# Kernel optimization log

Measured on AMD Instinct MI355X. Metric: run time of the kernel, lower is better.

## Reference

```python
import jax, jax.numpy as jnp
import numpy as np

B, M, K = 8, 2048, 2048
LAMBDA_VEL, LAMBDA_SURV, LAMBDA_OT = 1.0, 1.0, 0.1
REG_OT, REG_MASS, NUM_ITER_DIFF = 0.05, 1.0, 5


def setup_inputs() -> dict:
    key = jax.random.key(0)
    k0, k1, k2, k3, k4, k5 = jax.random.split(key, 6)
    return {
        "x_0": jax.random.normal(k0, (B, M, 3), jnp.float32),
        "x_gt": jax.random.normal(k1, (B, K, 3), jnp.float32),
        "v_pred": jax.random.normal(k2, (B, M, 3), jnp.float32),
        "alpha_pred": jax.random.normal(k3, (B, M, 1), jnp.float32),
        "t": jax.random.uniform(k4, (B, 1), jnp.float32),
        "matched_x_gt_precomputed": jax.random.normal(k5, (B, M, 3), jnp.float32),
    }


def _sinkhorn_unbalanced_log(log_a, log_b, K_log, tau, num_iter):
    # log_a: (B,M), log_b: (B,K), K_log: (B,M,K)
    log_u = jnp.zeros_like(log_a)
    log_v = jnp.zeros_like(log_b)
    for _ in range(num_iter):  # small fixed iteration count
        log_Kv = jax.nn.logsumexp(K_log + log_v[:, None, :], axis=2)   # (B,M)
        log_u = tau * (log_a - log_Kv)
        log_KTu = jax.nn.logsumexp(K_log + log_u[:, :, None], axis=1)  # (B,K)
        log_v = tau * (log_b - log_KTu)
    return jnp.exp(log_u[:, :, None] + K_log + log_v[:, None, :])      # pi (B,M,K)


def reference(x_0, x_gt, v_pred, alpha_pred, t, matched_x_gt_precomputed):
    sg = jax.lax.stop_gradient
    src = sg(x_0)   # (B,M,3)
    tgt = sg(x_gt)  # (B,K,3)

    # squared euclidean cost via gemm form (matches torch.cdist(p=2)**2)
    s2 = jnp.sum(src * src, axis=-1)  # (B,M)
    t2 = jnp.sum(tgt * tgt, axis=-1)  # (B,K)
    cost = s2[:, :, None] + t2[:, None, :] - 2.0 * jnp.einsum("bmd,bkd->bmk", src, tgt)
    cost = jnp.maximum(cost, 0.0)
    cost = cost / (jnp.max(cost, axis=(1, 2), keepdims=True) + 1e-8)

    # differentiable source marginal from survival logits
    alpha_soft = 10.0 * jnp.tanh(alpha_pred[..., 0] / 10.0)  # (B,M)
    a = jax.nn.sigmoid(alpha_soft)
    b = jnp.broadcast_to(jnp.sum(a, axis=1, keepdims=True) / K, (a.shape[0], K))

    tau = REG_MASS / (REG_MASS + REG_OT)
    log_a = jnp.log(jnp.maximum(a, 1e-30))
    log_b = jnp.log(jnp.maximum(b, 1e-30))
    K_log = -cost / REG_OT

    pi = _sinkhorn_unbalanced_log(log_a, log_b, K_log, tau, NUM_ITER_DIFF)  # (B,M,K)
    surv = jnp.sum(pi, axis=2)  # (B,M)
    surv_norm = jnp.clip(surv / (a + 1e-8), 0.0, 1.0)[..., None]  # (B,M,1)

    # velocity head
    v_target = sg(matched_x_gt_precomputed - x_0)
    weights = sg(jax.nn.sigmoid(alpha_pred))[..., 0]  # (B,M)
    sq_err = jnp.sum((v_pred - v_target) ** 2, axis=-1)
    loss_vel = jnp.sum(sq_err * weights) / jnp.maximum(jnp.sum(weights), 1.0)

    # survival head: BCE-with-logits, mean reduction
    x = alpha_pred
    y = sg(surv_norm)
    bce = jnp.maximum(x, 0.0) - x * y + jnp.log1p(jnp.exp(-jnp.abs(x)))
    loss_surv = jnp.mean(bce)

    # transport-cost head (differentiable through pi)
    loss_transport = jnp.sum(pi * sg(cost)) / jnp.maximum(jnp.sum(pi), 1e-8)

    return LAMBDA_VEL * loss_vel + LAMBDA_SURV * loss_surv + LAMBDA_OT * loss_transport
```

## Files before the change

### kernel.cpp

```cpp
#include <hip/hip_runtime.h>
#include <math.h>


#define LOG2E 1.4426950408889634f
#define TAU   0.95238095238095238f
#define NEG20LOG2E (-28.853900817779268f)

typedef float v2f __attribute__((ext_vector_type(2)));

enum : int {
  OFF_LU    = 0,
  OFF_LV    = 16384,
  OFF_CPART = 32768,
  OFF_SUMAP = 33280,
  OFF_SWP   = 33792,
  OFF_SEWP  = 34304,
  OFF_FPART = 34816,
  OFF_BBAR  = 36352,
  OFF_TAIL  = 40448,
  OFF_END   = 40480
};

__device__ __forceinline__ float fexp2(float x){ return __builtin_amdgcn_exp2f(x); }
__device__ __forceinline__ float flog2(float x){ return __builtin_amdgcn_logf(x); }

__device__ __forceinline__ float ld3(const float* p){
  return __hip_atomic_load(p, __ATOMIC_RELAXED, __HIP_MEMORY_SCOPE_AGENT);
}
__device__ __forceinline__ void st3(float* p, float v){
  __hip_atomic_store(p, v, __ATOMIC_RELAXED, __HIP_MEMORY_SCOPE_AGENT);
}

__device__ __forceinline__ float wave_sum(float v){
  #pragma unroll
  for(int m=32;m;m>>=1) v += __shfl_xor(v,m,64);
  return v;
}
__device__ __forceinline__ float wave_max(float v){
  #pragma unroll
  for(int m=32;m;m>>=1) v = fmaxf(v,__shfl_xor(v,m,64));
  return v;
}

__device__ __forceinline__ void bbar(unsigned* bbase, int phase, int blk){
  __syncthreads();
  if(threadIdx.x == 0){
    asm volatile("s_waitcnt vmcnt(0)" ::: "memory");
    const int g = (blk>>4)&3;
    unsigned* garr = bbase + g*32;
    unsigned* root = bbase + 4*32;
    unsigned* grel = bbase + (8+g)*32;
    const unsigned va = __hip_atomic_fetch_add(garr, 1u, __ATOMIC_RELAXED,
                                               __HIP_MEMORY_SCOPE_AGENT);
    if(va == (unsigned)(16*phase - 1)){
      const unsigned vr = __hip_atomic_fetch_add(root, 1u, __ATOMIC_RELAXED,
                                                 __HIP_MEMORY_SCOPE_AGENT);
      if(vr == (unsigned)(4*phase - 1)){
        #pragma unroll
        for(int g2=0; g2<4; ++g2)
          __hip_atomic_store(bbase + (8+g2)*32, (unsigned)phase,
                             __ATOMIC_RELAXED, __HIP_MEMORY_SCOPE_AGENT);
      }
    }
    while(__hip_atomic_load(grel, __ATOMIC_RELAXED, __HIP_MEMORY_SCOPE_AGENT)
          < (unsigned)phase)
      __builtin_amdgcn_s_sleep(1);
    asm volatile("" ::: "memory");
  }
  __syncthreads();
}

__global__ __launch_bounds__(256) void k_init(float* ws){
  unsigned* bar = reinterpret_cast<unsigned*>(ws);
  for(int i=threadIdx.x; i<OFF_END-OFF_BBAR; i+=256) bar[OFF_BBAR+i] = 0u;
}

#define LSE_PASS(ROWV, FIRSTV, PH) {                                          \
    const float4* sPT = ROWV ? sB : sA;                                       \
    float* lo = ws + (ROWV?OFF_LV:OFF_LU) + 2048*b;                           \
    float* op = ws + (ROWV?OFF_LU:OFF_LV);                                    \
    const float4 A0=ROWV?AR[0]:AC[0], A1=ROWV?AR[1]:AC[1],                    \
                 A2=ROWV?AR[2]:AC[2], A3=ROWV?AR[3]:AC[3];                    \
    if(!FIRSTV){                                                              \
      for(int i=tid;i<2048;i+=512) sL[i] = ld3(lo+i) + sPT[i].w;              \
    }                                                                         \
    __syncthreads();                                                          \
    const v2f ax01={A0.x,A1.x}, ay01={A0.y,A1.y}, az01={A0.z,A1.z};           \
    const v2f ax23={A2.x,A3.x}, ay23={A2.y,A3.y}, az23={A2.z,A3.z};           \
    v2f s01={0.0f,0.0f}, s23={0.0f,0.0f};                                     \
    _Pragma("unroll 2")                                                       \
    for(int k=lane;k<2048;k+=64){                                             \
      const float4 pt = sPT[k];                                               \
      const float wk = FIRSTV ? pt.w : sL[k];                                 \
      const v2f px={pt.x,pt.x}, py={pt.y,pt.y}, pz={pt.z,pt.z}, pw={wk,wk};   \
      const v2f c01 = __builtin_elementwise_fma(ax01,px,                      \
                      __builtin_elementwise_fma(ay01,py,                      \
                      __builtin_elementwise_fma(az01,pz,pw)));                \
      const v2f c23 = __builtin_elementwise_fma(ax23,px,                      \
                      __builtin_elementwise_fma(ay23,py,                      \
                      __builtin_elementwise_fma(az23,pz,pw)));                \
      s01 += (v2f){fexp2(c01.x), fexp2(c01.y)};                               \
      s23 += (v2f){fexp2(c23.x), fexp2(c23.y)};                               \
    }                                                                         \
    const float s0=wave_sum(s01.x), s1=wave_sum(s01.y);                       \
    const float s2=wave_sum(s23.x), s3=wave_sum(s23.y);                       \
    if(lane==0){                                                              \
      st3(op+r0g  , TAU*((ROWV?la[0]:lb2) - fmaf(sc,A0.w,flog2(s0))));        \
      st3(op+r0g+1, TAU*((ROWV?la[1]:lb2) - fmaf(sc,A1.w,flog2(s1))));        \
      st3(op+r0g+2, TAU*((ROWV?la[2]:lb2) - fmaf(sc,A2.w,flog2(s2))));        \
      st3(op+r0g+3, TAU*((ROWV?la[3]:lb2) - fmaf(sc,A3.w,flog2(s3))));        \
    }                                                                         \
    bbar(bbase, PH, blk);                                                     \
  }

__global__ __launch_bounds__(512,4) void k_fused(const float* __restrict__ x0,
                                                 const float* __restrict__ xgt,
                                                 const float* __restrict__ vp,
                                                 const float* __restrict__ ap,
                                                 const float* __restrict__ mxp,
                                                 float* __restrict__ ws,
                                                 float* __restrict__ out){
  __shared__ float4 sA[2048];
  __shared__ float4 sB[2048];
  __shared__ float  sL[2048];
  __shared__ float  sa32[32], sla[32], sal[32];
  __shared__ float  sred[24];
  __shared__ int    sLast;
  const int blk = blockIdx.x, tid = threadIdx.x, lane = tid&63, wid = tid>>6;
  const int b = blk>>6, j = blk&63;
  const int r0l = j*32 + (wid<<2);
  const int r0g = b*2048 + r0l;
  unsigned* bbase = reinterpret_cast<unsigned*>(ws) + OFF_BBAR + b*512;

  for(int i=tid;i<2048;i+=512){
    const int gi = (b*2048 + i)*3;
    const float x = x0[gi], y = x0[gi+1], z = x0[gi+2];
    sA[i] = make_float4(x,y,z, x*x+y*y+z*z);
    const float gx = xgt[gi], gy = xgt[gi+1], gz = xgt[gi+2];
    sB[i] = make_float4(gx,gy,gz, gx*gx+gy*gy+gz*gz);
  }
  if(wid == 0){
    float a_=0.0f, w_=0.0f, se_=0.0f;
    if(lane < 32){
      const int row = b*2048 + j*32 + lane;
      const float al = ap[row];
      const float a = 1.0f/(1.0f + fexp2(-10.0f*tanhf(al*0.1f)*LOG2E));
      sa32[lane] = a;
      sla[lane]  = flog2(fmaxf(a,1e-30f));
      sal[lane]  = al;
      const float w = 1.0f/(1.0f + fexp2(-al*LOG2E));
      const float x = x0[row*3], y = x0[row*3+1], z = x0[row*3+2];
      const float tx = mxp[row*3]-x, ty = mxp[row*3+1]-y, tz = mxp[row*3+2]-z;
      const float dx = vp[row*3]-tx, dy = vp[row*3+1]-ty, dz = vp[row*3+2]-tz;
      a_ = a; w_ = w; se_ = (dx*dx+dy*dy+dz*dz)*w;
    }
    const float sa_s = wave_sum(a_), sw_s = wave_sum(w_), sew_s = wave_sum(se_);
    if(lane == 0){
      st3(ws+OFF_SUMAP+blk, sa_s);
      st3(ws+OFF_SWP  +blk, sw_s);
      st3(ws+OFF_SEWP +blk, sew_s);
    }
  }
  __syncthreads();

  float4 AR[4], AC[4]; float la[4], av[4], alv[4];
  #pragma unroll
  for(int r=0;r<4;r++){
    AR[r] = sA[r0l+r]; AC[r] = sB[r0l+r];
    la[r] = sla[(wid<<2)+r]; av[r] = sa32[(wid<<2)+r]; alv[r] = sal[(wid<<2)+r];
  }

  {
    float c0=0,c1=0,c2=0,c3=0;
    #pragma unroll 2
    for(int k=lane;k<2048;k+=64){
      const float4 pt = sB[k];
      float d;
      d = AR[0].x*pt.x+AR[0].y*pt.y+AR[0].z*pt.z; c0=fmaxf(c0, AR[0].w+pt.w-2.0f*d);
      d = AR[1].x*pt.x+AR[1].y*pt.y+AR[1].z*pt.z; c1=fmaxf(c1, AR[1].w+pt.w-2.0f*d);
      d = AR[2].x*pt.x+AR[2].y*pt.y+AR[2].z*pt.z; c2=fmaxf(c2, AR[2].w+pt.w-2.0f*d);
      d = AR[3].x*pt.x+AR[3].y*pt.y+AR[3].z*pt.z; c3=fmaxf(c3, AR[3].w+pt.w-2.0f*d);
    }
    const float cmv = wave_max(fmaxf(fmaxf(c0,c1),fmaxf(c2,c3)));
    if(lane==0) sred[wid] = cmv;
    __syncthreads();
    if(tid==0){
      float m = sred[0];
      #pragma unroll
      for(int i=1;i<8;i++) m = fmaxf(m, sred[i]);
      st3(ws+OFF_CPART+blk, m);
    }
  }
  bbar(bbase, 1, blk);

  const float cm = wave_max(ld3(ws+OFF_CPART + b*64 + lane));
  const float sc = NEG20LOG2E/(cm + 1e-8f);
  const float n2sc = -2.0f*sc;
  const float sav = wave_sum(ld3(ws+OFF_SUMAP + b*64 + lane));
  const float lb2 = flog2(fmaxf(sav*(1.0f/2048.0f), 1e-30f));

  for(int i=tid;i<2048;i+=512){
    const float4 qa = sA[i];
    sA[i] = make_float4(n2sc*qa.x, n2sc*qa.y, n2sc*qa.z, sc*qa.w);
    const float4 qb = sB[i];
    sB[i] = make_float4(n2sc*qb.x, n2sc*qb.y, n2sc*qb.z, sc*qb.w);
  }
  __syncthreads();

  LSE_PASS(true,  true,  2)
  LSE_PASS(false, false, 3)
  LSE_PASS(true,  false, 4)
  LSE_PASS(false, false, 5)
  LSE_PASS(true,  false, 6)
  LSE_PASS(false, false, 7)
  LSE_PASS(true,  false, 8)
  LSE_PASS(false, false, 9)
  LSE_PASS(true,  false, 10)
  LSE_PASS(false, false, 11)

  {
    float* lv = ws + OFF_LV + 2048*b;
    for(int i=tid;i<2048;i+=512) sL[i] = ld3(lv+i);
    __syncthreads();
    const float lu0=ld3(ws+OFF_LU+r0g),   lu1=ld3(ws+OFF_LU+r0g+1);
    const float lu2=ld3(ws+OFF_LU+r0g+2), lu3=ld3(ws+OFF_LU+r0g+3);
    const v2f ax01={AR[0].x,AR[1].x}, ay01={AR[0].y,AR[1].y}, az01={AR[0].z,AR[1].z};
    const v2f ax23={AR[2].x,AR[3].x}, ay23={AR[2].y,AR[3].y}, az23={AR[2].z,AR[3].z};
    v2f S01={0.0f,0.0f},S23={0.0f,0.0f};
    v2f Q01={0.0f,0.0f},Q23={0.0f,0.0f};
    v2f L01={0.0f,0.0f},L23={0.0f,0.0f};
    #pragma unroll 2
    for(int k=lane;k<2048;k+=64){
      const float4 pt = sB[k];
      const float lvk = sL[k];
      const float wk = pt.w + lvk;
      const v2f px={pt.x,pt.x}, py={pt.y,pt.y}, pz={pt.z,pt.z}, pw={wk,wk};
      const v2f lk={lvk,lvk};
      const v2f c01 = __builtin_elementwise_fma(ax01,px,
                      __builtin_elementwise_fma(ay01,py,
                      __builtin_elementwise_fma(az01,pz,pw)));
      const v2f c23 = __builtin_elementwise_fma(ax23,px,
                      __builtin_elementwise_fma(ay23,py,
                      __builtin_elementwise_fma(az23,pz,pw)));
      const v2f p01 = {fexp2(c01.x), fexp2(c01.y)};
      const v2f p23 = {fexp2(c23.x), fexp2(c23.y)};
      S01 += p01;                      S23 += p23;
      Q01 = __builtin_elementwise_fma(p01,c01,Q01);
      Q23 = __builtin_elementwise_fma(p23,c23,Q23);
      L01 = __builtin_elementwise_fma(p01,lk,L01);
      L23 = __builtin_elementwise_fma(p23,lk,L23);
    }
    float S[4]={wave_sum(S01.x),wave_sum(S01.y),wave_sum(S23.x),wave_sum(S23.y)};
    float Q[4]={wave_sum(Q01.x),wave_sum(Q01.y),wave_sum(Q23.x),wave_sum(Q23.y)};
    float L[4]={wave_sum(L01.x),wave_sum(L01.y),wave_sum(L23.x),wave_sum(L23.y)};
    const float lus[4]={lu0,lu1,lu2,lu3};
    float spc = 0.0f, bce = 0.0f, spt = 0.0f;
    #pragma unroll
    for(int r=0;r<4;r++){
      const float cr = fmaf(sc, AR[r].w, lus[r]);
      const float p2 = fexp2(cr);
      const float sp = p2*S[r];
      spc += p2*fmaf(cr,S[r],Q[r]) - p2*L[r] - lus[r]*sp;
      float yv = sp / (av[r] + 1e-8f);
      yv = fminf(fmaxf(yv,0.0f),1.0f);
      const float al = alv[r];
      bce += fmaxf(al,0.0f) - al*yv
           + 0.69314718056f*flog2(1.0f + fexp2(-fabsf(al)*LOG2E));
      spt += sp;
    }
    if(lane==0){ sred[wid]=bce; sred[8+wid]=spt; sred[16+wid]=spc; }
    __syncthreads();
    if(tid==0){
      float tb=0, ts=0, tc=0;
      #pragma unroll
      for(int i=0;i<8;i++){ tb+=sred[i]; ts+=sred[8+i]; tc+=sred[16+i]; }
      st3(ws+OFF_FPART +        blk, tb);
      st3(ws+OFF_FPART + 512  + blk, ts);
      st3(ws+OFF_FPART + 1024 + blk, tc);
    }
  }

  __syncthreads();
  if(tid == 0){
    asm volatile("s_waitcnt vmcnt(0)" ::: "memory");
    unsigned* tail = reinterpret_cast<unsigned*>(ws) + OFF_TAIL;
    const unsigned v = __hip_atomic_fetch_add(tail, 1u, __ATOMIC_RELAXED,
                                              __HIP_MEMORY_SCOPE_AGENT);
    sLast = (v == 511u) ? 1 : 0;
  }
  __syncthreads();
  if(sLast){
    float pb = ld3(ws+OFF_FPART+tid);
    float ps = ld3(ws+OFF_FPART+512+tid);
    float pc = ld3(ws+OFF_FPART+1024+tid);
    float pw = ld3(ws+OFF_SWP+tid);
    float pe = ld3(ws+OFF_SEWP+tid);
    pb=wave_sum(pb); ps=wave_sum(ps); pc=wave_sum(pc);
    pw=wave_sum(pw); pe=wave_sum(pe);
    if(lane==0){
      sL[wid*5+0]=pb; sL[wid*5+1]=ps; sL[wid*5+2]=pc;
      sL[wid*5+3]=pw; sL[wid*5+4]=pe;
    }
    __syncthreads();
    if(tid==0){
      float bce=0, sp=0, spc=0, sw=0, sew=0;
      #pragma unroll
      for(int w=0;w<8;w++){
        bce+=sL[w*5+0]; sp+=sL[w*5+1]; spc+=sL[w*5+2];
        sw +=sL[w*5+3]; sew+=sL[w*5+4];
      }
      const float loss_vel  = sew / fmaxf(sw, 1.0f);
      const float loss_surv = bce / 16384.0f;
      const float loss_tr = (spc * (-0.03465735902799726f)) / fmaxf(sp, 1e-8f);
      out[0] = loss_vel + loss_surv + 0.1f*loss_tr;
    }
  }
}

extern "C" void kernel_launch(void* const* d_in, const int* in_sizes, int n_in,
                              void* d_out, int out_size, void* d_ws, size_t ws_size,
                              hipStream_t stream) {
  (void)in_sizes; (void)n_in; (void)out_size; (void)ws_size;
  const float* x0  = (const float*)d_in[0];
  const float* xgt = (const float*)d_in[1];
  const float* vp  = (const float*)d_in[2];
  const float* ap  = (const float*)d_in[3];
  const float* mxp = (const float*)d_in[5];
  float* ws  = (float*)d_ws;
  float* out = (float*)d_out;

  k_init<<<1, 256, 0, stream>>>(ws);

  k_fused<<<512, 512, 0, stream>>>(x0, xgt, vp, ap, mxp, ws, out);
}
```

Before: 108.8 us.

## Switch shared point storage to SoA pairs and vectorize over columns

```diff
diff --git a/kernel.cpp b/kernel.cpp
--- a/kernel.cpp
+++ b/kernel.cpp
@@ -23,6 +23,9 @@
 
 __device__ __forceinline__ float fexp2(float x){ return __builtin_amdgcn_exp2f(x); }
 __device__ __forceinline__ float flog2(float x){ return __builtin_amdgcn_logf(x); }
+__device__ __forceinline__ v2f vfma(v2f a, v2f b, v2f c){
+  return __builtin_elementwise_fma(a,b,c);
+}
 
 __device__ __forceinline__ float ld3(const float* p){
   return __hip_atomic_load(p, __ATOMIC_RELAXED, __HIP_MEMORY_SCOPE_AGENT);
@@ -76,39 +79,44 @@
 }
 
 #define LSE_PASS(ROWV, FIRSTV, PH) {                                          \
-    const float4* sPT = ROWV ? sB : sA;                                       \
+    const v2f* SX = ROWV ? sxB : sxA;                                         \
+    const v2f* SY = ROWV ? syB : syA;                                         \
+    const v2f* SZ = ROWV ? szB : szA;                                         \
+    const v2f* SN = ROWV ? n2B : n2A;                                         \
+    const float4* AF = ROWV ? AR : AC;                                        \
     float* lo = ws + (ROWV?OFF_LV:OFF_LU) + 2048*b;                           \
     float* op = ws + (ROWV?OFF_LU:OFF_LV);                                    \
-    const float4 A0=ROWV?AR[0]:AC[0], A1=ROWV?AR[1]:AC[1],                    \
-                 A2=ROWV?AR[2]:AC[2], A3=ROWV?AR[3]:AC[3];                    \
-    if(!FIRSTV){                                                              \
-      for(int i=tid;i<2048;i+=512) sL[i] = ld3(lo+i) + sPT[i].w;              \
+    for(int s=tid;s<1024;s+=512){                                             \
+      const v2f pot = FIRSTV ? (v2f){0.0f,0.0f}                               \
+                             : (v2f){ld3(lo+2*s), ld3(lo+2*s+1)};             \
+      swf[s] = SN[s] + pot;                                                   \
     }                                                                         \
     __syncthreads();                                                          \
-    const v2f ax01={A0.x,A1.x}, ay01={A0.y,A1.y}, az01={A0.z,A1.z};           \
-    const v2f ax23={A2.x,A3.x}, ay23={A2.y,A3.y}, az23={A2.z,A3.z};           \
-    v2f s01={0.0f,0.0f}, s23={0.0f,0.0f};                                     \
+    const v2f ax0={AF[0].x,AF[0].x}, ay0={AF[0].y,AF[0].y}, az0={AF[0].z,AF[0].z};\
+    const v2f ax1={AF[1].x,AF[1].x}, ay1={AF[1].y,AF[1].y}, az1={AF[1].z,AF[1].z};\
+    const v2f ax2={AF[2].x,AF[2].x}, ay2={AF[2].y,AF[2].y}, az2={AF[2].z,AF[2].z};\
+    const v2f ax3={AF[3].x,AF[3].x}, ay3={AF[3].y,AF[3].y}, az3={AF[3].z,AF[3].z};\
+    float sl0=0,sh0=0,sl1=0,sh1=0,sl2=0,sh2=0,sl3=0,sh3=0;                    \
     _Pragma("unroll 2")                                                       \
-    for(int k=lane;k<2048;k+=64){                                             \
-      const float4 pt = sPT[k];                                               \
-      const float wk = FIRSTV ? pt.w : sL[k];                                 \
-      const v2f px={pt.x,pt.x}, py={pt.y,pt.y}, pz={pt.z,pt.z}, pw={wk,wk};   \
-      const v2f c01 = __builtin_elementwise_fma(ax01,px,                      \
-                      __builtin_elementwise_fma(ay01,py,                      \
-                      __builtin_elementwise_fma(az01,pz,pw)));                \
-      const v2f c23 = __builtin_elementwise_fma(ax23,px,                      \
-                      __builtin_elementwise_fma(ay23,py,                      \
-                      __builtin_elementwise_fma(az23,pz,pw)));                \
-      s01 += (v2f){fexp2(c01.x), fexp2(c01.y)};                               \
-      s23 += (v2f){fexp2(c23.x), fexp2(c23.y)};                               \
+    for(int p=lane;p<1024;p+=64){                                             \
+      const v2f xp=SX[p], yp=SY[p], zp=SZ[p], wp=swf[p];                      \
+      v2f c;                                                                  \
+      c = vfma(ax0,xp,vfma(ay0,yp,vfma(az0,zp,wp)));                          \
+      sl0 += fexp2(c[0]); sh0 += fexp2(c[1]);                                 \
+      c = vfma(ax1,xp,vfma(ay1,yp,vfma(az1,zp,wp)));                          \
+      sl1 += fexp2(c[0]); sh1 += fexp2(c[1]);                                 \
+      c = vfma(ax2,xp,vfma(ay2,yp,vfma(az2,zp,wp)));                          \
+      sl2 += fexp2(c[0]); sh2 += fexp2(c[1]);                                 \
+      c = vfma(ax3,xp,vfma(ay3,yp,vfma(az3,zp,wp)));                          \
+      sl3 += fexp2(c[0]); sh3 += fexp2(c[1]);                                 \
     }                                                                         \
-    const float s0=wave_sum(s01.x), s1=wave_sum(s01.y);                       \
-    const float s2=wave_sum(s23.x), s3=wave_sum(s23.y);                       \
+    const float s0=wave_sum(sl0+sh0), s1=wave_sum(sl1+sh1);                   \
+    const float s2=wave_sum(sl2+sh2), s3=wave_sum(sl3+sh3);                   \
     if(lane==0){                                                              \
-      st3(op+r0g  , TAU*((ROWV?la[0]:lb2) - fmaf(sc,A0.w,flog2(s0))));        \
-      st3(op+r0g+1, TAU*((ROWV?la[1]:lb2) - fmaf(sc,A1.w,flog2(s1))));        \
-      st3(op+r0g+2, TAU*((ROWV?la[2]:lb2) - fmaf(sc,A2.w,flog2(s2))));        \
-      st3(op+r0g+3, TAU*((ROWV?la[3]:lb2) - fmaf(sc,A3.w,flog2(s3))));        \
+      st3(op+r0g  , TAU*((ROWV?la[0]:lb2) - fmaf(sc,AF[0].w,flog2(s0))));     \
+      st3(op+r0g+1, TAU*((ROWV?la[1]:lb2) - fmaf(sc,AF[1].w,flog2(s1))));     \
+      st3(op+r0g+2, TAU*((ROWV?la[2]:lb2) - fmaf(sc,AF[2].w,flog2(s2))));     \
+      st3(op+r0g+3, TAU*((ROWV?la[3]:lb2) - fmaf(sc,AF[3].w,flog2(s3))));     \
     }                                                                         \
     bbar(bbase, PH, blk);                                                     \
   }
@@ -120,24 +128,28 @@
                                                  const float* __restrict__ mxp,
                                                  float* __restrict__ ws,
                                                  float* __restrict__ out){
-  __shared__ float4 sA[2048];
-  __shared__ float4 sB[2048];
-  __shared__ float  sL[2048];
-  __shared__ float  sa32[32], sla[32], sal[32];
-  __shared__ float  sred[24];
-  __shared__ int    sLast;
+  __shared__ v2f sxA[1024], syA[1024], szA[1024], n2A[1024];
+  __shared__ v2f sxB[1024], syB[1024], szB[1024], n2B[1024];
+  __shared__ v2f swf[1024];
+  __shared__ float sa32[32], sla[32], sal[32];
+  __shared__ float sred[24];
+  __shared__ int   sLast;
   const int blk = blockIdx.x, tid = threadIdx.x, lane = tid&63, wid = tid>>6;
   const int b = blk>>6, j = blk&63;
   const int r0l = j*32 + (wid<<2);
   const int r0g = b*2048 + r0l;
   unsigned* bbase = reinterpret_cast<unsigned*>(ws) + OFF_BBAR + b*512;
 
-  for(int i=tid;i<2048;i+=512){
-    const int gi = (b*2048 + i)*3;
-    const float x = x0[gi], y = x0[gi+1], z = x0[gi+2];
-    sA[i] = make_float4(x,y,z, x*x+y*y+z*z);
-    const float gx = xgt[gi], gy = xgt[gi+1], gz = xgt[gi+2];
-    sB[i] = make_float4(gx,gy,gz, gx*gx+gy*gy+gz*gz);
+  for(int s=tid;s<1024;s+=512){
+    const int gi = (b*2048 + 2*s)*3;
+    const float xa0=x0[gi],  ya0=x0[gi+1], za0=x0[gi+2];
+    const float xa1=x0[gi+3],ya1=x0[gi+4], za1=x0[gi+5];
+    sxA[s]=(v2f){xa0,xa1}; syA[s]=(v2f){ya0,ya1}; szA[s]=(v2f){za0,za1};
+    n2A[s]=(v2f){xa0*xa0+ya0*ya0+za0*za0, xa1*xa1+ya1*ya1+za1*za1};
+    const float xb0=xgt[gi],  yb0=xgt[gi+1], zb0=xgt[gi+2];
+    const float xb1=xgt[gi+3],yb1=xgt[gi+4], zb1=xgt[gi+5];
+    sxB[s]=(v2f){xb0,xb1}; syB[s]=(v2f){yb0,yb1}; szB[s]=(v2f){zb0,zb1};
+    n2B[s]=(v2f){xb0*xb0+yb0*yb0+zb0*zb0, xb1*xb1+yb1*yb1+zb1*zb1};
   }
   if(wid == 0){
     float a_=0.0f, w_=0.0f, se_=0.0f;
@@ -163,24 +175,36 @@
   }
   __syncthreads();
 
+  const float* fxA = (const float*)sxA; const float* fyA = (const float*)syA;
+  const float* fzA = (const float*)szA; const float* fnA = (const float*)n2A;
+  const float* fxB = (const float*)sxB; const float* fyB = (const float*)syB;
+  const float* fzB = (const float*)szB; const float* fnB = (const float*)n2B;
   float4 AR[4], AC[4]; float la[4], av[4], alv[4];
   #pragma unroll
   for(int r=0;r<4;r++){
-    AR[r] = sA[r0l+r]; AC[r] = sB[r0l+r];
+    const int q = r0l + r;
+    AR[r] = make_float4(fxA[q], fyA[q], fzA[q], fnA[q]);
+    AC[r] = make_float4(fxB[q], fyB[q], fzB[q], fnB[q]);
     la[r] = sla[(wid<<2)+r]; av[r] = sa32[(wid<<2)+r]; alv[r] = sal[(wid<<2)+r];
   }
 
   {
-    float c0=0,c1=0,c2=0,c3=0;
+    const v2f h0x={-2*AR[0].x,-2*AR[0].x}, h0y={-2*AR[0].y,-2*AR[0].y}, h0z={-2*AR[0].z,-2*AR[0].z};
+    const v2f h1x={-2*AR[1].x,-2*AR[1].x}, h1y={-2*AR[1].y,-2*AR[1].y}, h1z={-2*AR[1].z,-2*AR[1].z};
+    const v2f h2x={-2*AR[2].x,-2*AR[2].x}, h2y={-2*AR[2].y,-2*AR[2].y}, h2z={-2*AR[2].z,-2*AR[2].z};
+    const v2f h3x={-2*AR[3].x,-2*AR[3].x}, h3y={-2*AR[3].y,-2*AR[3].y}, h3z={-2*AR[3].z,-2*AR[3].z};
+    float m0=-1e30f,m1=-1e30f,m2=-1e30f,m3=-1e30f;
     #pragma unroll 2
-    for(int k=lane;k<2048;k+=64){
-      const float4 pt = sB[k];
-      float d;
-      d = AR[0].x*pt.x+AR[0].y*pt.y+AR[0].z*pt.z; c0=fmaxf(c0, AR[0].w+pt.w-2.0f*d);
-      d = AR[1].x*pt.x+AR[1].y*pt.y+AR[1].z*pt.z; c1=fmaxf(c1, AR[1].w+pt.w-2.0f*d);
-      d = AR[2].x*pt.x+AR[2].y*pt.y+AR[2].z*pt.z; c2=fmaxf(c2, AR[2].w+pt.w-2.0f*d);
-      d = AR[3].x*pt.x+AR[3].y*pt.y+AR[3].z*pt.z; c3=fmaxf(c3, AR[3].w+pt.w-2.0f*d);
-    }
+    for(int p=lane;p<1024;p+=64){
+      const v2f xp=sxB[p], yp=syB[p], zp=szB[p], np=n2B[p];
+      v2f c;
+      c = vfma(h0x,xp,vfma(h0y,yp,vfma(h0z,zp,np))); m0=fmaxf(m0,fmaxf(c[0],c[1]));
+      c = vfma(h1x,xp,vfma(h1y,yp,vfma(h1z,zp,np))); m1=fmaxf(m1,fmaxf(c[0],c[1]));
+      c = vfma(h2x,xp,vfma(h2y,yp,vfma(h2z,zp,np))); m2=fmaxf(m2,fmaxf(c[0],c[1]));
+      c = vfma(h3x,xp,vfma(h3y,yp,vfma(h3z,zp,np))); m3=fmaxf(m3,fmaxf(c[0],c[1]));
+    }
+    const float c0 = fmaxf(0.0f, AR[0].w + m0), c1 = fmaxf(0.0f, AR[1].w + m1);
+    const float c2 = fmaxf(0.0f, AR[2].w + m2), c3 = fmaxf(0.0f, AR[3].w + m3);
     const float cmv = wave_max(fmaxf(fmaxf(c0,c1),fmaxf(c2,c3)));
     if(lane==0) sred[wid] = cmv;
     __syncthreads();
@@ -199,11 +223,12 @@
   const float sav = wave_sum(ld3(ws+OFF_SUMAP + b*64 + lane));
   const float lb2 = flog2(fmaxf(sav*(1.0f/2048.0f), 1e-30f));
 
-  for(int i=tid;i<2048;i+=512){
-    const float4 qa = sA[i];
-    sA[i] = make_float4(n2sc*qa.x, n2sc*qa.y, n2sc*qa.z, sc*qa.w);
-    const float4 qb = sB[i];
-    sB[i] = make_float4(n2sc*qb.x, n2sc*qb.y, n2sc*qb.z, sc*qb.w);
+  {
+    const v2f vs = {n2sc, n2sc}, vc = {sc, sc};
+    for(int s=tid;s<1024;s+=512){
+      sxA[s]*=vs; syA[s]*=vs; szA[s]*=vs; n2A[s]*=vc;
+      sxB[s]*=vs; syB[s]*=vs; szB[s]*=vs; n2B[s]*=vc;
+    }
   }
   __syncthreads();
 
@@ -220,47 +245,50 @@
 
   {
     float* lv = ws + OFF_LV + 2048*b;
-    for(int i=tid;i<2048;i+=512) sL[i] = ld3(lv+i);
+    for(int s=tid;s<1024;s+=512)
+      swf[s] = n2B[s] + (v2f){ld3(lv+2*s), ld3(lv+2*s+1)};
     __syncthreads();
-    const float lu0=ld3(ws+OFF_LU+r0g),   lu1=ld3(ws+OFF_LU+r0g+1);
-    const float lu2=ld3(ws+OFF_LU+r0g+2), lu3=ld3(ws+OFF_LU+r0g+3);
-    const v2f ax01={AR[0].x,AR[1].x}, ay01={AR[0].y,AR[1].y}, az01={AR[0].z,AR[1].z};
-    const v2f ax23={AR[2].x,AR[3].x}, ay23={AR[2].y,AR[3].y}, az23={AR[2].z,AR[3].z};
-    v2f S01={0.0f,0.0f},S23={0.0f,0.0f};
-    v2f Q01={0.0f,0.0f},Q23={0.0f,0.0f};
-    v2f L01={0.0f,0.0f},L23={0.0f,0.0f};
+    const v2f ax0={AR[0].x,AR[0].x}, ay0={AR[0].y,AR[0].y}, az0={AR[0].z,AR[0].z};
+    const v2f ax1={AR[1].x,AR[1].x}, ay1={AR[1].y,AR[1].y}, az1={AR[1].z,AR[1].z};
+    const v2f ax2={AR[2].x,AR[2].x}, ay2={AR[2].y,AR[2].y}, az2={AR[2].z,AR[2].z};
+    const v2f ax3={AR[3].x,AR[3].x}, ay3={AR[3].y,AR[3].y}, az3={AR[3].z,AR[3].z};
+    float S[4]={0,0,0,0}, Q[4]={0,0,0,0}, Pw[4]={0,0,0,0}, P2[4]={0,0,0,0};
     #pragma unroll 2
-    for(int k=lane;k<2048;k+=64){
-      const float4 pt = sB[k];
-      const float lvk = sL[k];
-      const float wk = pt.w + lvk;
-      const v2f px={pt.x,pt.x}, py={pt.y,pt.y}, pz={pt.z,pt.z}, pw={wk,wk};
-      const v2f lk={lvk,lvk};
-      const v2f c01 = __builtin_elementwise_fma(ax01,px,
-                      __builtin_elementwise_fma(ay01,py,
-                      __builtin_elementwise_fma(az01,pz,pw)));
-      const v2f c23 = __builtin_elementwise_fma(ax23,px,
-                      __builtin_elementwise_fma(ay23,py,
-                      __builtin_elementwise_fma(az23,pz,pw)));
-      const v2f p01 = {fexp2(c01.x), fexp2(c01.y)};
-      const v2f p23 = {fexp2(c23.x), fexp2(c23.y)};
-      S01 += p01;                      S23 += p23;
-      Q01 = __builtin_elementwise_fma(p01,c01,Q01);
-      Q23 = __builtin_elementwise_fma(p23,c23,Q23);
-      L01 = __builtin_elementwise_fma(p01,lk,L01);
-      L23 = __builtin_elementwise_fma(p23,lk,L23);
-    }
-    float S[4]={wave_sum(S01.x),wave_sum(S01.y),wave_sum(S23.x),wave_sum(S23.y)};
-    float Q[4]={wave_sum(Q01.x),wave_sum(Q01.y),wave_sum(Q23.x),wave_sum(Q23.y)};
-    float L[4]={wave_sum(L01.x),wave_sum(L01.y),wave_sum(L23.x),wave_sum(L23.y)};
-    const float lus[4]={lu0,lu1,lu2,lu3};
+    for(int p=lane;p<1024;p+=64){
+      const v2f xp=sxB[p], yp=syB[p], zp=szB[p], wp=swf[p], np=n2B[p];
+      v2f c; float e0, e1;
+      c = vfma(ax0,xp,vfma(ay0,yp,vfma(az0,zp,wp)));
+      e0=fexp2(c[0]); e1=fexp2(c[1]);
+      S[0]+=e0+e1; Q[0]=fmaf(e0,c[0],fmaf(e1,c[1],Q[0]));
+      Pw[0]=fmaf(e0,wp[0],fmaf(e1,wp[1],Pw[0]));
+      P2[0]=fmaf(e0,np[0],fmaf(e1,np[1],P2[0]));
+      c = vfma(ax1,xp,vfma(ay1,yp,vfma(az1,zp,wp)));
+      e0=fexp2(c[0]); e1=fexp2(c[1]);
+      S[1]+=e0+e1; Q[1]=fmaf(e0,c[0],fmaf(e1,c[1],Q[1]));
+      Pw[1]=fmaf(e0,wp[0],fmaf(e1,wp[1],Pw[1]));
+      P2[1]=fmaf(e0,np[0],fmaf(e1,np[1],P2[1]));
+      c = vfma(ax2,xp,vfma(ay2,yp,vfma(az2,zp,wp)));
+      e0=fexp2(c[0]); e1=fexp2(c[1]);
+      S[2]+=e0+e1; Q[2]=fmaf(e0,c[0],fmaf(e1,c[1],Q[2]));
+      Pw[2]=fmaf(e0,wp[0],fmaf(e1,wp[1],Pw[2]));
+      P2[2]=fmaf(e0,np[0],fmaf(e1,np[1],P2[2]));
+      c = vfma(ax3,xp,vfma(ay3,yp,vfma(az3,zp,wp)));
+      e0=fexp2(c[0]); e1=fexp2(c[1]);
+      S[3]+=e0+e1; Q[3]=fmaf(e0,c[0],fmaf(e1,c[1],Q[3]));
+      Pw[3]=fmaf(e0,wp[0],fmaf(e1,wp[1],Pw[3]));
+      P2[3]=fmaf(e0,np[0],fmaf(e1,np[1],P2[3]));
+    }
     float spc = 0.0f, bce = 0.0f, spt = 0.0f;
     #pragma unroll
     for(int r=0;r<4;r++){
-      const float cr = fmaf(sc, AR[r].w, lus[r]);
+      const float St = wave_sum(S[r]);
+      const float Qt = wave_sum(Q[r]);
+      const float Lt = wave_sum(Pw[r]) - wave_sum(P2[r]);
+      const float lur = ld3(ws+OFF_LU+r0g+r);
+      const float cr = fmaf(sc, AR[r].w, lur);
       const float p2 = fexp2(cr);
-      const float sp = p2*S[r];
-      spc += p2*fmaf(cr,S[r],Q[r]) - p2*L[r] - lus[r]*sp;
+      const float sp = p2*St;
+      spc += p2*fmaf(cr,St,Qt) - p2*Lt - lur*sp;
       float yv = sp / (av[r] + 1e-8f);
       yv = fminf(fmaxf(yv,0.0f),1.0f);
       const float al = alv[r];
@@ -297,6 +325,7 @@
     float pe = ld3(ws+OFF_SEWP+tid);
     pb=wave_sum(pb); ps=wave_sum(ps); pc=wave_sum(pc);
     pw=wave_sum(pw); pe=wave_sum(pe);
+    float* sL = (float*)swf;
     if(lane==0){
       sL[wid*5+0]=pb; sL[wid*5+1]=ps; sL[wid*5+2]=pc;
       sL[wid*5+3]=pw; sL[wid*5+4]=pe;
```

Result: faster. 100.5 us (-7.6%).
